# Optimization experiments

Measured on AMD Instinct MI355X. Metric: run time of the kernel, lower is better.

Reference implementation:

```python
import jax, jax.numpy as jnp
import numpy as np

FILTER_LENGTHS = (2, 4)  # from module: self.filter_length = [2, 4]


def _get_conv(signal, b, h, l, d_k, conv, w):
    # signal: [b, h*d_k, l] (raw reshape of [b,h,l,d_k], matching torch .reshape)
    f = max(FILTER_LENGTHS)
    pad = f // 2
    padded = jnp.pad(signal, ((0, 0), (0, 0), (pad, pad)))  # [b, d, l+f]
    # unfold(-1, f, 1)[:, :, :l, :] -> sliding windows, keep first l
    idx = jnp.arange(l)[:, None] + jnp.arange(f)[None, :]  # [l, f]
    seq = padded[:, :, idx]  # [b, d, l, f]
    # dynamic filter-length selection: w_f = filter_lengths * w, pick argmax
    f_s = jnp.asarray(FILTER_LENGTHS, dtype=signal.dtype)
    ind = jnp.argmax(f_s * w)
    chosen_len = jnp.asarray(FILTER_LENGTHS)[ind]
    mask = (jnp.arange(f) < chosen_len).astype(signal.dtype)  # [f]
    seq = seq * mask  # broadcast over [b, d, l, f]
    # depthwise-ish conv via einsum, then raw reshape (b, l, h*d_k) -> (b, h, l, d_k)
    out = jnp.einsum('bdlf,dof->blo', seq, conv)
    return out.reshape(b, h, l, d_k)


def reference(Q, K, V, attn_mask, conv_q, conv_k, w):
    b, h, l, d_k = Q.shape
    Qc = _get_conv(Q.reshape(b, h * d_k, l), b, h, l, d_k, conv_q, w) + Q
    Kc = _get_conv(K.reshape(b, h * d_k, l), b, h, l, d_k, conv_k, w) + K
    scores = jnp.einsum('bhqd,bhkd->bhqk', Qc, Kc) / np.sqrt(d_k).astype(Q.dtype)
    attn = jax.nn.softmax(scores, axis=-1)
    context = jnp.einsum('bhqk,bhkd->bhqd', attn, V)
    return context, attn


def setup_inputs() -> dict:
    key = jax.random.key(0)
    ks = jax.random.split(key, 6)
    b, h, l, d_k = 4, 8, 2048, 64
    d = h * d_k
    f = max(FILTER_LENGTHS)
    return {
        'Q': jax.random.normal(ks[0], (b, h, l, d_k), dtype=jnp.float32),
        'K': jax.random.normal(ks[1], (b, h, l, d_k), dtype=jnp.float32),
        'V': jax.random.normal(ks[2], (b, h, l, d_k), dtype=jnp.float32),
        'attn_mask': jnp.zeros((b, 1, l, l), dtype=bool),  # unused by forward
        'conv_q': jax.random.normal(ks[3], (d, d, f), dtype=jnp.float32),
        'conv_k': jax.random.normal(ks[4], (d, d, f), dtype=jnp.float32),
        'w': jax.random.normal(ks[5], (2,), dtype=jnp.float32),
    }
```

## Files before the change

kernel.cpp:

```cpp
#include <hip/hip_runtime.h>

typedef _Float16 f16;
typedef _Float16 f16x4 __attribute__((ext_vector_type(4)));
typedef _Float16 f16x8 __attribute__((ext_vector_type(8)));
typedef float f32x4 __attribute__((ext_vector_type(4)));
typedef float f32x16 __attribute__((ext_vector_type(16)));

#define MFMA32(A, B, C) __builtin_amdgcn_mfma_f32_32x32x16_f16(A, B, C, 0, 0, 0)

constexpr int Bb = 4, Hh = 8, Ll = 2048, Dk = 64, Dm = 512, BH = 32;

constexpr size_t NWF = (size_t)16 * 128 * 64 * 8;
constexpr size_t NAF = (size_t)Bb * 64 * 128 * 64 * 8;
constexpr size_t NFF = (size_t)BH * 64 * 4 * 64 * 8;
constexpr size_t NVF = (size_t)BH * 2 * 128 * 64 * 8;

constexpr size_t OFF_WF = 256;
constexpr size_t OFF_AF = OFF_WF + 4 * NWF * sizeof(f16);
constexpr size_t OFF_FF = OFF_AF + 4 * NAF * sizeof(f16);
constexpr size_t OFF_VF = OFF_FF + 4 * NFF * sizeof(f16);

#define QSCALE 0.1803368801111204f

__global__ void kprep_w(const float* __restrict__ convq, const float* __restrict__ convk,
                        const float* __restrict__ w, int* __restrict__ flag,
                        f16* __restrict__ wfhq, f16* __restrict__ wflq,
                        f16* __restrict__ wfhk, f16* __restrict__ wflk) {
    const int len = (4.f * w[1] > 2.f * w[0]) ? 4 : 2;
    if (blockIdx.x == 0 && blockIdx.y == 0 && threadIdx.x == 0) *flag = len;
    int g = blockIdx.x * 256 + threadIdx.x;
    int o = g & 511, c8 = g >> 9;
    const float* conv = blockIdx.y ? convk : convq;
    f16* dh = blockIdx.y ? wfhk : wfhq;
    f16* dl = blockIdx.y ? wflk : wflq;
    float4 v[8];
#pragma unroll
    for (int cc = 0; cc < 8; ++cc)
        v[cc] = *(const float4*)(conv + ((size_t)(c8 * 8 + cc) * 512 + o) * 4);
    int ob = o >> 5;
#pragma unroll
    for (int f = 0; f < 4; ++f) {
        f16x8 hv, lv;
#pragma unroll
        for (int cc = 0; cc < 8; ++cc) {
            float x = (f < len) ? ((const float*)&v[cc])[f] : 0.f;
            f16 hi = (f16)x;
            hv[cc] = hi; lv[cc] = (f16)(x - (float)hi);
        }
        int k16 = f * 32 + (c8 >> 1);
        size_t base = (((size_t)ob * 128 + k16) * 64 + (c8 & 1) * 32 + (o & 31)) * 8;
        *(f16x8*)(dh + base) = hv;
        *(f16x8*)(dl + base) = lv;
    }
}

__global__ void kprep_a(const float* __restrict__ Q, const float* __restrict__ K,
                        const int* __restrict__ flag,
                        f16* __restrict__ afhq, f16* __restrict__ aflq,
                        f16* __restrict__ afhk, f16* __restrict__ aflk) {
    __shared__ float tile[64][36];
    int tensor = blockIdx.z, b = blockIdx.y;
    int tb = blockIdx.x >> 3, crange = blockIdx.x & 7;
    int c0 = crange * 64;
    const int flen = *flag;
    const float* S = (tensor ? K : Q) + (size_t)b * Dm * Ll;
    int tid = threadIdx.x;
    int t0 = tb * 32;
#pragma unroll
    for (int i = 0; i < 9; ++i) {
        int e = i * 256 + tid;
        int row = e / 36, col = e - row * 36;
        int t = t0 - 2 + col;
        tile[row][col] = (t >= 0 && t < Ll) ? S[(size_t)(c0 + row) * Ll + t] : 0.f;
    }
    __syncthreads();
    int sub = tid >> 6, lane = tid & 63;
    int khalf = lane >> 5, lane31 = lane & 31;
    f16* dh = tensor ? afhk : afhq;
    f16* dl = tensor ? aflk : aflq;
    for (int f = 0; f < flen; ++f) {
        int k16 = (f * 8 + crange) * 4 + sub;
        f16x8 hv, lv;
#pragma unroll
        for (int j = 0; j < 8; ++j) {
            int cl = sub * 16 + khalf * 8 + j;
            float x = tile[cl][lane31 + f];
            f16 hi = (f16)x;
            hv[j] = hi; lv[j] = (f16)(x - (float)hi);
        }
        size_t idx = ((((size_t)b * 64 + tb) * 128 + k16) * 64 + lane) * 8;
        *(f16x8*)(dh + idx) = hv;
        *(f16x8*)(dl + idx) = lv;
    }
}

__global__ void kprep_v(const float* __restrict__ V, f16* __restrict__ vf) {
    int bh = blockIdx.y, l0 = blockIdx.x * 128;
    int tid = threadIdx.x;
    const float* src = V + (size_t)bh * Ll * Dk;
#pragma unroll
    for (int s = 0; s < 4; ++s) {
        int g = s * 4 + (tid >> 6);
        int lane = tid & 63;
        int l16s = g >> 1, db = g & 1;
        int khalf = lane >> 5, lane31 = lane & 31;
        int d = db * 32 + lane31;
        f16x8 out;
#pragma unroll
        for (int j = 0; j < 8; ++j) {
            int l = l0 + l16s * 16 + khalf * 8 + j;
            out[j] = (f16)src[(size_t)l * Dk + d];
        }
        size_t idx = ((((size_t)bh * 2 + db) * 128 + (l0 >> 4) + l16s) * 64 + lane) * 8;
        *(f16x8*)(vf + idx) = out;
    }
}

__global__ __launch_bounds__(256, 4) void kconv(
    const float* __restrict__ Q, const float* __restrict__ K, const int* __restrict__ flag,
    const f16* __restrict__ afhq, const f16* __restrict__ aflq,
    const f16* __restrict__ afhk, const f16* __restrict__ aflk,
    const f16* __restrict__ wfhq, const f16* __restrict__ wflq,
    const f16* __restrict__ wfhk, const f16* __restrict__ wflk,
    f16* __restrict__ ffhq, f16* __restrict__ fflq,
    f16* __restrict__ ffhk, f16* __restrict__ fflk) {
    int id = blockIdx.x;
    int xcd = id & 7, oTile = (id >> 3) & 3, gidx = id >> 5;
    int g = gidx * 8 + xcd;
    int tt = g & 31, b = (g >> 5) & 3, tensor = (g >> 7) & 1;
    int wave = threadIdx.x >> 6, lane = threadIdx.x & 63;
    int wn = wave & 1, wm = wave >> 1;
    int lane31 = lane & 31, khalf = lane >> 5;
    const f16* ah = (tensor ? afhk : afhq) + ((size_t)(b * 64 + tt * 2 + wm) * 128) * 512;
    const f16* al = (tensor ? aflk : aflq) + ((size_t)(b * 64 + tt * 2 + wm) * 128) * 512;
    const f16* bhp = (tensor ? wfhk : wfhq) + ((size_t)(oTile * 4 + wn * 2) * 128) * 512;
    const f16* blp = (tensor ? wflk : wflq) + ((size_t)(oTile * 4 + wn * 2) * 128) * 512;
    const float* src = (tensor ? K : Q) + (size_t)b * Hh * Ll * Dk;
    f16* dh = (tensor ? ffhk : ffhq);
    f16* dl = (tensor ? fflk : fflq);
    const float scale = tensor ? 1.f : QSCALE;
    const int klen16 = (*flag) << 5;

    f32x16 acc[2];
#pragma unroll
    for (int j = 0; j < 2; ++j)
#pragma unroll
        for (int r = 0; r < 16; ++r) acc[j][r] = 0.f;

    f16x8 Aah, Aal, Abh[2], Abl[2];
    f16x8 Bah, Bal, Bbh[2], Bbl[2];
    const size_t lo8 = (size_t)lane * 8;

    Aah = *(const f16x8*)(ah + lo8);
    Aal = *(const f16x8*)(al + lo8);
    Abh[0] = *(const f16x8*)(bhp + lo8);
    Abl[0] = *(const f16x8*)(blp + lo8);
    Abh[1] = *(const f16x8*)(bhp + 128 * 512 + lo8);
    Abl[1] = *(const f16x8*)(blp + 128 * 512 + lo8);

    for (int k16 = 0; k16 < klen16; k16 += 2) {
        {
            int kn = k16 + 1 < klen16 ? k16 + 1 : k16;
            size_t o = (size_t)kn * 512 + lo8;
            Bah = *(const f16x8*)(ah + o);
            Bal = *(const f16x8*)(al + o);
            Bbh[0] = *(const f16x8*)(bhp + o);
            Bbl[0] = *(const f16x8*)(blp + o);
            Bbh[1] = *(const f16x8*)(bhp + 128 * 512 + o);
            Bbl[1] = *(const f16x8*)(blp + 128 * 512 + o);
        }
#pragma unroll
        for (int j = 0; j < 2; ++j) {
            acc[j] = MFMA32(Aah, Abh[j], acc[j]);
            acc[j] = MFMA32(Aah, Abl[j], acc[j]);
            acc[j] = MFMA32(Aal, Abh[j], acc[j]);
        }
        {
            int kn = k16 + 2 < klen16 ? k16 + 2 : klen16 - 1;
            size_t o = (size_t)kn * 512 + lo8;
            Aah = *(const f16x8*)(ah + o);
            Aal = *(const f16x8*)(al + o);
            Abh[0] = *(const f16x8*)(bhp + o);
            Abl[0] = *(const f16x8*)(blp + o);
            Abh[1] = *(const f16x8*)(bhp + 128 * 512 + o);
            Abl[1] = *(const f16x8*)(blp + 128 * 512 + o);
        }
#pragma unroll
        for (int j = 0; j < 2; ++j) {
            acc[j] = MFMA32(Bah, Bbh[j], acc[j]);
            acc[j] = MFMA32(Bah, Bbl[j], acc[j]);
            acc[j] = MFMA32(Bal, Bbh[j], acc[j]);
        }
    }
#pragma unroll
    for (int j = 0; j < 2; ++j)
#pragma unroll
        for (int r = 0; r < 16; ++r) {
            int trow = tt * 64 + wm * 32 + (r & 3) + ((r >> 2) << 3) + (khalf << 2);
            int ocol = oTile * 128 + wn * 64 + j * 32 + lane31;
            int h = trow >> 8;
            int l = ((trow & 255) << 3) + (ocol >> 6);
            int d = ocol & 63;
            float v2 = (acc[j][r] + src[((size_t)h * Ll + l) * Dk + d]) * scale;
            f16 hi = (f16)v2;
            f16 lo = (f16)(v2 - (float)hi);
            size_t idx = ((((size_t)(b * 8 + h) * 64 + (l >> 5)) * 4 + (d >> 4)) * 64
                          + ((d >> 3) & 1) * 32 + (l & 31)) * 8 + (d & 7);
            dh[idx] = hi; dl[idx] = lo;
        }
}

#define LOADK(DST, CH) do { size_t kb_ = (size_t)(CH) * 2048 + lane * 8;            \
    _Pragma("unroll") for (int ks_ = 0; ks_ < 4; ++ks_) {                           \
        DST[2 * ks_]     = *(const f16x8*)(kbh + kb_ + ks_ * 512);                  \
        DST[2 * ks_ + 1] = *(const f16x8*)(kbl + kb_ + ks_ * 512); } } while (0)

#define QKM(SRC, ACC) do { _Pragma("unroll") for (int ks_ = 0; ks_ < 4; ++ks_) {    \
        ACC = MFMA32(a_h[ks_], SRC[2 * ks_], ACC);                                  \
        ACC = MFMA32(a_h[ks_], SRC[2 * ks_ + 1], ACC);                              \
        ACC = MFMA32(a_l[ks_], SRC[2 * ks_], ACC); } } while (0)

#define SMUPD(ACC) do { _Pragma("unroll") for (int r_ = 0; r_ < 16; ++r_) {         \
        float v_ = ACC[r_]; float d_ = v_ - m[r_]; float e_ = exp2f(-fabsf(d_));    \
        bool gt_ = d_ > 0.f;                                                        \
        s[r_] = gt_ ? __fmaf_rn(s[r_], e_, 1.f) : (s[r_] + e_);                     \
        m[r_] = gt_ ? v_ : m[r_]; } } while (0)

#define LOADV(DST, CH) do { _Pragma("unroll") for (int q_ = 0; q_ < 4; ++q_) {      \
        int n_ = q_ >> 1, ks2_ = q_ & 1;                                            \
        size_t off_ = ((((size_t)bh * 2 + n_) * 128 + (CH) * 2 + ks2_) * 64 + lane) * 8; \
        DST[q_] = *(const f16x8*)(vf + off_); } } while (0)

union SMemU {
    float combuf[2][32][64];
    f16 sbuf[4][32][264];
};

__global__ __launch_bounds__(256, 2) void kattn(
    const f16* __restrict__ qfh, const f16* __restrict__ qfl,
    const f16* __restrict__ kfh, const f16* __restrict__ kfl,
    const f16* __restrict__ vf,
    float* __restrict__ ctx_out, float* __restrict__ attn_out) {
    __shared__ __align__(16) SMemU sm;
    int id = blockIdx.x;
    int bh = (id & 7) * 4 + (id >> 8);
    int qt = (id >> 3) & 31;
    int wave = threadIdx.x >> 6, lane = threadIdx.x & 63;
    int qg = wave >> 1, kg = wave & 1;
    int lane31 = lane & 31, khalf = lane >> 5;
    int q0 = qt * 64 + qg * 32;

    f16x8 a_h[4], a_l[4];
    {
        size_t qb = ((size_t)bh * 64 + qt * 2 + qg) * 4;
#pragma unroll
        for (int ks = 0; ks < 4; ++ks) {
            a_h[ks] = *(const f16x8*)(qfh + ((qb + ks) * 64 + lane) * 8);
            a_l[ks] = *(const f16x8*)(qfl + ((qb + ks) * 64 + lane) * 8);
        }
    }
    const f16* kbh = kfh + (size_t)bh * 131072;
    const f16* kbl = kfl + (size_t)bh * 131072;
    const int ch0 = kg * 32, ch1 = ch0 + 32;

    float m[16], s[16];
#pragma unroll
    for (int r = 0; r < 16; ++r) { m[r] = -3.0e38f; s[r] = 0.f; }

    {
        f16x8 KA[8], KB[8];
        LOADK(KA, ch0);
        for (int ch = ch0; ch < ch1; ch += 2) {
            LOADK(KB, ch + 1);
            f32x16 acc;
#pragma unroll
            for (int r = 0; r < 16; ++r) acc[r] = 0.f;
            QKM(KA, acc);
            SMUPD(acc);
            {
                int chn = (ch + 2 < ch1) ? ch + 2 : ch;
                LOADK(KA, chn);
            }
            f32x16 acc2;
#pragma unroll
            for (int r = 0; r < 16; ++r) acc2[r] = 0.f;
            QKM(KB, acc2);
            SMUPD(acc2);
        }
    }
#pragma unroll
    for (int r = 0; r < 16; ++r) {
        float mm = m[r], ss = s[r];
#pragma unroll
        for (int off = 1; off < 32; off <<= 1) {
            float mo = __shfl_xor(mm, off, 64);
            float so = __shfl_xor(ss, off, 64);
            float mn = fmaxf(mm, mo);
            ss = ss * exp2f(mm - mn) + so * exp2f(mo - mn);
            mm = mn;
        }
        m[r] = mm; s[r] = ss;
    }
    if (kg == 1) {
#pragma unroll
        for (int r = 0; r < 16; ++r) {
            sm.combuf[qg][r][lane] = m[r];
            sm.combuf[qg][16 + r][lane] = s[r];
        }
    }
    __syncthreads();
    if (kg == 0) {
#pragma unroll
        for (int r = 0; r < 16; ++r) {
            float m1 = sm.combuf[qg][r][lane];
            float s1 = sm.combuf[qg][16 + r][lane];
            float mn = fmaxf(m[r], m1);
            float ss = s[r] * exp2f(m[r] - mn) + s1 * exp2f(m1 - mn);
            m[r] = mn; s[r] = 1.f / ss;
            sm.combuf[qg][r][lane] = mn;
            sm.combuf[qg][16 + r][lane] = s[r];
        }
    }
    __syncthreads();
    if (kg == 1) {
#pragma unroll
        for (int r = 0; r < 16; ++r) {
            m[r] = sm.combuf[qg][r][lane];
            s[r] = sm.combuf[qg][16 + r][lane];
        }
    }
    __syncthreads();

    f32x16 ctx[2];
#pragma unroll
    for (int n = 0; n < 2; ++n)
#pragma unroll
        for (int r = 0; r < 16; ++r) ctx[n][r] = 0.f;

    const size_t rowbase = ((size_t)bh * Ll + q0) * Ll;

    {
        f16x8 KV[8], VV[4];
        LOADK(KV, ch0);
        LOADV(VV, ch0);
        for (int chb = ch0; chb < ch1; chb += 8) {
#pragma unroll
            for (int i = 0; i < 8; ++i) {
                int ch = chb + i;
                f32x16 acc;
#pragma unroll
                for (int r = 0; r < 16; ++r) acc[r] = 0.f;
                QKM(KV, acc);
                int chn = (ch + 1 < ch1) ? ch + 1 : ch;
                LOADK(KV, chn);
#pragma unroll
                for (int r = 0; r < 16; ++r) {
                    float p = exp2f(acc[r] - m[r]) * s[r];
                    int row = (r & 3) + ((r >> 2) << 3) + (khalf << 2);
                    sm.sbuf[wave][row][i * 32 + lane31] = (f16)p;
                }
                __asm__ volatile("s_waitcnt lgkmcnt(0)" ::: "memory");
#pragma unroll
                for (int ks2 = 0; ks2 < 2; ++ks2) {
                    f16x8 pa = *(const f16x8*)&sm.sbuf[wave][lane31][i * 32 + ks2 * 16 + khalf * 8];
                    ctx[0] = MFMA32(pa, VV[ks2], ctx[0]);
                    ctx[1] = MFMA32(pa, VV[2 + ks2], ctx[1]);
                }
                LOADV(VV, chn);
            }
#pragma unroll
            for (int ri = 0; ri < 16; ++ri) {
                int row = ri * 2 + khalf;
                f16x8 pv = *(const f16x8*)&sm.sbuf[wave][row][lane31 * 8];
                f32x4 o0 = {(float)pv[0], (float)pv[1], (float)pv[2], (float)pv[3]};
                f32x4 o1 = {(float)pv[4], (float)pv[5], (float)pv[6], (float)pv[7]};
                float* dst = attn_out + rowbase + (size_t)row * Ll + chb * 32 + lane31 * 8;
                *(f32x4*)dst = o0;
                *(f32x4*)(dst + 4) = o1;
            }
        }
    }
    __syncthreads();
    if (kg == 1) {
#pragma unroll
        for (int n = 0; n < 2; ++n)
#pragma unroll
            for (int r = 0; r < 16; ++r) sm.combuf[qg][n * 16 + r][lane] = ctx[n][r];
    }
    __syncthreads();
    if (kg == 0) {
#pragma unroll
        for (int n = 0; n < 2; ++n)
#pragma unroll
            for (int r = 0; r < 16; ++r) {
                float v = ctx[n][r] + sm.combuf[qg][n * 16 + r][lane];
                int row = (r & 3) + ((r >> 2) << 3) + (khalf << 2);
                ctx_out[((size_t)bh * Ll + q0 + row) * Dk + n * 32 + lane31] = v;
            }
    }
}

extern "C" void kernel_launch(void* const* d_in, const int* in_sizes, int n_in,
                              void* d_out, int out_size, void* d_ws, size_t ws_size,
                              hipStream_t stream) {
    const float* Q = (const float*)d_in[0];
    const float* K = (const float*)d_in[1];
    const float* V = (const float*)d_in[2];
    const float* convq = (const float*)d_in[4];
    const float* convk = (const float*)d_in[5];
    const float* w = (const float*)d_in[6];

    char* ws = (char*)d_ws;
    int* flag = (int*)ws;
    f16* wfhq = (f16*)(ws + OFF_WF);
    f16* wflq = wfhq + NWF;
    f16* wfhk = wflq + NWF;
    f16* wflk = wfhk + NWF;
    f16* afhq = (f16*)(ws + OFF_AF);
    f16* aflq = afhq + NAF;
    f16* afhk = aflq + NAF;
    f16* aflk = afhk + NAF;
    f16* ffhq = (f16*)(ws + OFF_FF);
    f16* fflq = ffhq + NFF;
    f16* ffhk = fflq + NFF;
    f16* fflk = ffhk + NFF;
    f16* vf = (f16*)(ws + OFF_VF);

    float* ctx_out = (float*)d_out;
    float* attn_out = ctx_out + (size_t)BH * Ll * Dk;

    kprep_w<<<dim3(128, 2), 256, 0, stream>>>(convq, convk, w, flag, wfhq, wflq, wfhk, wflk);
    kprep_v<<<dim3(16, 32), 256, 0, stream>>>(V, vf);
    kprep_a<<<dim3(512, 4, 2), 256, 0, stream>>>(Q, K, flag, afhq, aflq, afhk, aflk);
    kconv<<<dim3(1024), 256, 0, stream>>>(Q, K, flag, afhq, aflq, afhk, aflk,
                                          wfhq, wflq, wfhk, wflk, ffhq, fflq, ffhk, fflk);
    kattn<<<dim3(1024), 256, 0, stream>>>(ffhq, fflq, ffhk, fflk, vf, ctx_out, attn_out);
}
```

Measured before the change: 993.9 us.

## Fuse activation unfold and fp16 split into conv GEMM, drop kprep_a

Removes the kprep_a kernel that materialised the unfolded, hi/lo-split fp16 activation operand in workspace. The conv kernel now gathers raw fp32 Q/K values straight from global memory, with clamped time indices and a zero mask for the padding, and converts them to hi/lo fp16 in registers before the MFMAs. This saves one launch and a large write-then-read of the split activation buffer. In exchange the inner loop issues strided scalar global loads (stride Ll per element) that are uncoalesced across channels and may be reloaded by several blocks.

```diff
diff --git a/kernel.cpp b/kernel.cpp
--- a/kernel.cpp
+++ b/kernel.cpp
@@ -11,13 +11,11 @@
 constexpr int Bb = 4, Hh = 8, Ll = 2048, Dk = 64, Dm = 512, BH = 32;
 
 constexpr size_t NWF = (size_t)16 * 128 * 64 * 8;
-constexpr size_t NAF = (size_t)Bb * 64 * 128 * 64 * 8;
 constexpr size_t NFF = (size_t)BH * 64 * 4 * 64 * 8;
 constexpr size_t NVF = (size_t)BH * 2 * 128 * 64 * 8;
 
 constexpr size_t OFF_WF = 256;
-constexpr size_t OFF_AF = OFF_WF + 4 * NWF * sizeof(f16);
-constexpr size_t OFF_FF = OFF_AF + 4 * NAF * sizeof(f16);
+constexpr size_t OFF_FF = OFF_WF + 4 * NWF * sizeof(f16);
 constexpr size_t OFF_VF = OFF_FF + 4 * NFF * sizeof(f16);
 
 #define QSCALE 0.1803368801111204f
@@ -54,46 +52,6 @@
     }
 }
 
-__global__ void kprep_a(const float* __restrict__ Q, const float* __restrict__ K,
-                        const int* __restrict__ flag,
-                        f16* __restrict__ afhq, f16* __restrict__ aflq,
-                        f16* __restrict__ afhk, f16* __restrict__ aflk) {
-    __shared__ float tile[64][36];
-    int tensor = blockIdx.z, b = blockIdx.y;
-    int tb = blockIdx.x >> 3, crange = blockIdx.x & 7;
-    int c0 = crange * 64;
-    const int flen = *flag;
-    const float* S = (tensor ? K : Q) + (size_t)b * Dm * Ll;
-    int tid = threadIdx.x;
-    int t0 = tb * 32;
-#pragma unroll
-    for (int i = 0; i < 9; ++i) {
-        int e = i * 256 + tid;
-        int row = e / 36, col = e - row * 36;
-        int t = t0 - 2 + col;
-        tile[row][col] = (t >= 0 && t < Ll) ? S[(size_t)(c0 + row) * Ll + t] : 0.f;
-    }
-    __syncthreads();
-    int sub = tid >> 6, lane = tid & 63;
-    int khalf = lane >> 5, lane31 = lane & 31;
-    f16* dh = tensor ? afhk : afhq;
-    f16* dl = tensor ? aflk : aflq;
-    for (int f = 0; f < flen; ++f) {
-        int k16 = (f * 8 + crange) * 4 + sub;
-        f16x8 hv, lv;
-#pragma unroll
-        for (int j = 0; j < 8; ++j) {
-            int cl = sub * 16 + khalf * 8 + j;
-            float x = tile[cl][lane31 + f];
-            f16 hi = (f16)x;
-            hv[j] = hi; lv[j] = (f16)(x - (float)hi);
-        }
-        size_t idx = ((((size_t)b * 64 + tb) * 128 + k16) * 64 + lane) * 8;
-        *(f16x8*)(dh + idx) = hv;
-        *(f16x8*)(dl + idx) = lv;
-    }
-}
-
 __global__ void kprep_v(const float* __restrict__ V, f16* __restrict__ vf) {
     int bh = blockIdx.y, l0 = blockIdx.x * 128;
     int tid = threadIdx.x;
@@ -118,8 +76,6 @@
 
 __global__ __launch_bounds__(256, 4) void kconv(
     const float* __restrict__ Q, const float* __restrict__ K, const int* __restrict__ flag,
-    const f16* __restrict__ afhq, const f16* __restrict__ aflq,
-    const f16* __restrict__ afhk, const f16* __restrict__ aflk,
     const f16* __restrict__ wfhq, const f16* __restrict__ wflq,
     const f16* __restrict__ wfhk, const f16* __restrict__ wflk,
     f16* __restrict__ ffhq, f16* __restrict__ fflq,
@@ -131,15 +87,15 @@
     int wave = threadIdx.x >> 6, lane = threadIdx.x & 63;
     int wn = wave & 1, wm = wave >> 1;
     int lane31 = lane & 31, khalf = lane >> 5;
-    const f16* ah = (tensor ? afhk : afhq) + ((size_t)(b * 64 + tt * 2 + wm) * 128) * 512;
-    const f16* al = (tensor ? aflk : aflq) + ((size_t)(b * 64 + tt * 2 + wm) * 128) * 512;
     const f16* bhp = (tensor ? wfhk : wfhq) + ((size_t)(oTile * 4 + wn * 2) * 128) * 512;
     const f16* blp = (tensor ? wflk : wflq) + ((size_t)(oTile * 4 + wn * 2) * 128) * 512;
-    const float* src = (tensor ? K : Q) + (size_t)b * Hh * Ll * Dk;
+    const float* src = (tensor ? K : Q) + (size_t)b * Dm * Ll;
     f16* dh = (tensor ? ffhk : ffhq);
     f16* dl = (tensor ? fflk : fflq);
     const float scale = tensor ? 1.f : QSCALE;
     const int klen16 = (*flag) << 5;
+    const int t0 = (tt * 2 + wm) * 32;
+    const int coff = khalf * 8;
 
     f32x16 acc[2];
 #pragma unroll
@@ -147,12 +103,27 @@
 #pragma unroll
         for (int r = 0; r < 16; ++r) acc[j][r] = 0.f;
 
-    f16x8 Aah, Aal, Abh[2], Abl[2];
-    f16x8 Bah, Bal, Bbh[2], Bbl[2];
+    f16x8 Abh[2], Abl[2], Bbh[2], Bbl[2];
+    float XA[8], XB[8], mkA, mkB;
     const size_t lo8 = (size_t)lane * 8;
 
-    Aah = *(const f16x8*)(ah + lo8);
-    Aal = *(const f16x8*)(al + lo8);
+#define LOADX(X, MK, KN) do {                                                        \
+    int f_ = (KN) >> 5;                                                              \
+    int cb_ = (((KN) >> 2) & 7) * 64 + ((KN) & 3) * 16 + coff;                       \
+    int t_ = t0 - 2 + lane31 + f_;                                                   \
+    int tc_ = t_ < 0 ? 0 : (t_ > Ll - 1 ? Ll - 1 : t_);                              \
+    MK = (t_ == tc_) ? 1.f : 0.f;                                                    \
+    const float* sp_ = src + (size_t)cb_ * Ll + tc_;                                 \
+    _Pragma("unroll") for (int j_ = 0; j_ < 8; ++j_) X[j_] = sp_[(size_t)j_ * Ll];   \
+} while (0)
+
+#define CVTA(X, MK, AH, AL) do {                                                     \
+    _Pragma("unroll") for (int j_ = 0; j_ < 8; ++j_) {                               \
+        float x_ = X[j_] * MK; f16 h_ = (f16)x_;                                     \
+        AH[j_] = h_; AL[j_] = (f16)(x_ - (float)h_); }                               \
+} while (0)
+
+    LOADX(XA, mkA, 0);
     Abh[0] = *(const f16x8*)(bhp + lo8);
     Abl[0] = *(const f16x8*)(blp + lo8);
     Abh[1] = *(const f16x8*)(bhp + 128 * 512 + lo8);
@@ -160,38 +131,46 @@
 
     for (int k16 = 0; k16 < klen16; k16 += 2) {
         {
-            int kn = k16 + 1 < klen16 ? k16 + 1 : k16;
+            int kn = k16 + 1;
+            LOADX(XB, mkB, kn);
             size_t o = (size_t)kn * 512 + lo8;
-            Bah = *(const f16x8*)(ah + o);
-            Bal = *(const f16x8*)(al + o);
             Bbh[0] = *(const f16x8*)(bhp + o);
             Bbl[0] = *(const f16x8*)(blp + o);
             Bbh[1] = *(const f16x8*)(bhp + 128 * 512 + o);
             Bbl[1] = *(const f16x8*)(blp + 128 * 512 + o);
         }
-#pragma unroll
-        for (int j = 0; j < 2; ++j) {
-            acc[j] = MFMA32(Aah, Abh[j], acc[j]);
-            acc[j] = MFMA32(Aah, Abl[j], acc[j]);
-            acc[j] = MFMA32(Aal, Abh[j], acc[j]);
+        {
+            f16x8 Ah, Al;
+            CVTA(XA, mkA, Ah, Al);
+#pragma unroll
+            for (int j = 0; j < 2; ++j) {
+                acc[j] = MFMA32(Ah, Abh[j], acc[j]);
+                acc[j] = MFMA32(Ah, Abl[j], acc[j]);
+                acc[j] = MFMA32(Al, Abh[j], acc[j]);
+            }
         }
         {
             int kn = k16 + 2 < klen16 ? k16 + 2 : klen16 - 1;
+            LOADX(XA, mkA, kn);
             size_t o = (size_t)kn * 512 + lo8;
-            Aah = *(const f16x8*)(ah + o);
-            Aal = *(const f16x8*)(al + o);
             Abh[0] = *(const f16x8*)(bhp + o);
             Abl[0] = *(const f16x8*)(blp + o);
             Abh[1] = *(const f16x8*)(bhp + 128 * 512 + o);
             Abl[1] = *(const f16x8*)(blp + 128 * 512 + o);
         }
-#pragma unroll
-        for (int j = 0; j < 2; ++j) {
-            acc[j] = MFMA32(Bah, Bbh[j], acc[j]);
-            acc[j] = MFMA32(Bah, Bbl[j], acc[j]);
-            acc[j] = MFMA32(Bal, Bbh[j], acc[j]);
-        }
-    }
+        {
+            f16x8 Bh, Bl;
+            CVTA(XB, mkB, Bh, Bl);
+#pragma unroll
+            for (int j = 0; j < 2; ++j) {
+                acc[j] = MFMA32(Bh, Bbh[j], acc[j]);
+                acc[j] = MFMA32(Bh, Bbl[j], acc[j]);
+                acc[j] = MFMA32(Bl, Bbh[j], acc[j]);
+            }
+        }
+    }
+#undef LOADX
+#undef CVTA
 #pragma unroll
     for (int j = 0; j < 2; ++j)
 #pragma unroll
@@ -416,10 +395,6 @@
     f16* wflq = wfhq + NWF;
     f16* wfhk = wflq + NWF;
     f16* wflk = wfhk + NWF;
-    f16* afhq = (f16*)(ws + OFF_AF);
-    f16* aflq = afhq + NAF;
-    f16* afhk = aflq + NAF;
-    f16* aflk = afhk + NAF;
     f16* ffhq = (f16*)(ws + OFF_FF);
     f16* fflq = ffhq + NFF;
     f16* ffhk = fflq + NFF;
@@ -431,8 +406,7 @@
 
     kprep_w<<<dim3(128, 2), 256, 0, stream>>>(convq, convk, w, flag, wfhq, wflq, wfhk, wflk);
     kprep_v<<<dim3(16, 32), 256, 0, stream>>>(V, vf);
-    kprep_a<<<dim3(512, 4, 2), 256, 0, stream>>>(Q, K, flag, afhq, aflq, afhk, aflk);
-    kconv<<<dim3(1024), 256, 0, stream>>>(Q, K, flag, afhq, aflq, afhk, aflk,
+    kconv<<<dim3(1024), 256, 0, stream>>>(Q, K, flag,
                                           wfhq, wflq, wfhk, wflk, ffhq, fflq, ffhk, fflk);
     kattn<<<dim3(1024), 256, 0, stream>>>(ffhq, fflq, ffhk, fflk, vf, ctx_out, attn_out);
 }
```

Result: faster. 973.9 us (-2.0%).
